# Kernel tuning notes

Hardware: AMD Instinct MI355X
Metric: run time of the kernel (lower is better)

The kernel has to match this reference:

```python
import jax, jax.numpy as jnp
import numpy as np

Q, N, FDIM, HDIM = 4096, 1024, 64, 128


def setup_inputs() -> dict:
    key = jax.random.key(0)
    ks = jax.random.split(key, 7)
    s = 0.05
    return {
        "query_points": jax.random.normal(ks[0], (Q, 3), dtype=jnp.float32),
        "node_features": jax.random.normal(ks[1], (N, FDIM), dtype=jnp.float32),
        "node_positions": jax.random.normal(ks[2], (N, 3), dtype=jnp.float32),
        # attention MLP: Linear(F+3 -> H), ReLU, Linear(H -> 1)
        "aW1": jax.random.normal(ks[3], (FDIM + 3, HDIM), dtype=jnp.float32) * s,
        "ab1": jnp.zeros((HDIM,), dtype=jnp.float32),
        "aW2": jax.random.normal(ks[4], (HDIM, 1), dtype=jnp.float32) * s,
        "ab2": jnp.zeros((1,), dtype=jnp.float32),
        # decoder MLP: Linear(F -> H), ReLU, Linear(H -> 3)
        "dW1": jax.random.normal(ks[5], (FDIM, HDIM), dtype=jnp.float32) * s,
        "db1": jnp.zeros((HDIM,), dtype=jnp.float32),
        "dW2": jax.random.normal(ks[6], (HDIM, 3), dtype=jnp.float32) * s,
        "db2": jnp.zeros((3,), dtype=jnp.float32),
    }


def reference(query_points, node_features, node_positions,
              aW1, ab1, aW2, ab2, dW1, db1, dW2, db2):
    F = node_features.shape[1]
    # pairwise offsets: [Q, N, 3]
    diff = query_points[:, None, :] - node_positions[None, :, :]
    # xy-plane distance -> inverse-distance weights: [Q, N, 1]
    dist = jnp.linalg.norm(diff[..., :2], axis=-1, keepdims=True)
    w = 1.0 / (dist + 1e-6)
    # attn MLP on concat([node_features, diff]); split W1 so the feature
    # part ([N,F]@[F,H]) is computed once instead of per query pair.
    h = jax.nn.relu(node_features @ aW1[:F] + diff @ aW1[F:] + ab1)  # [Q, N, H]
    score = h @ aW2 + ab2                                            # [Q, N, 1]
    attn = jax.nn.softmax(score * w, axis=1)                         # [Q, N, 1]
    agg = jnp.einsum('qn,nf->qf', attn[..., 0], node_features)       # [Q, F]
    return jax.nn.relu(agg @ dW1 + db1) @ dW2 + db2                  # [Q, 3]
```

## Files before the change

kernel.cpp:

```cpp
#include <hip/hip_runtime.h>
#include <math.h>

#define QN 4096
#define NN 1024
#define FD 64
#define HD 128

typedef float v2f __attribute__((ext_vector_type(2)));

#define OFF_UT2   0
#define OFF_B     524288
#define OFF_VU    655360
#define OFF_VB    659456
#define OFF_L     660480
#define OFF_PM    4854784
#define OFF_PART  5116928
#define OFF_SPART 7214080

__global__ __launch_bounds__(256) void k0_prep(
    const float* __restrict__ qp, const float* __restrict__ nf,
    const float* __restrict__ npos, const float* __restrict__ aW1,
    const float* __restrict__ ab1, const float* __restrict__ aW2,
    float* __restrict__ B, float* __restrict__ UT2,
    float* __restrict__ vu, float* __restrict__ vb) {
  int bid = blockIdx.x, t = threadIdx.x;
  if (bid < 2048) {
    int idx = bid * 256 + t;
    int e = idx & 1, q = (idx >> 1) & 4095, h2 = idx >> 13;
    int h = h2 * 2 + e;
    float u = qp[q*3+0] * aW1[(FD+0)*HD + h]
            + qp[q*3+1] * aW1[(FD+1)*HD + h]
            + qp[q*3+2] * aW1[(FD+2)*HD + h];
    UT2[idx] = u;
  } else if (bid < 2560) {
    int i2 = (bid - 2048) * 256 + t;
    int n = i2 >> 7, h = i2 & 127;
    float s = ab1[h];
    #pragma unroll
    for (int f = 0; f < FD; ++f) s = fmaf(nf[n*FD+f], aW1[f*HD+h], s);
    s -= npos[n*3+0] * aW1[(FD+0)*HD + h]
       + npos[n*3+1] * aW1[(FD+1)*HD + h]
       + npos[n*3+2] * aW1[(FD+2)*HD + h];
    B[i2] = s;
    float pv = s * aW2[h];
    #pragma unroll
    for (int m = 1; m < 64; m <<= 1) pv += __shfl_xor(pv, m, 64);
    __shared__ float ps[4];
    if ((t & 63) == 0) ps[t >> 6] = pv;
    __syncthreads();
    if (t == 0)   vb[n] = ps[0] + ps[1];
    if (t == 128) vb[n] = ps[2] + ps[3];
  } else {
    int q = (bid - 2560) * 256 + t;
    float q0 = qp[q*3+0], q1 = qp[q*3+1], q2 = qp[q*3+2];
    float acc = 0.f;
    #pragma unroll
    for (int h = 0; h < HD; ++h) {
      float u = q0 * aW1[(FD+0)*HD + h]
              + q1 * aW1[(FD+1)*HD + h]
              + q2 * aW1[(FD+2)*HD + h];
      acc = fmaf(aW2[h], u, acc);
    }
    vu[q] = acc;
  }
}

__global__ __launch_bounds__(256) void k2_logits(
    const float* __restrict__ Bg, const float* __restrict__ UT2,
    const float* __restrict__ aW2, const float* __restrict__ ab2,
    const float* __restrict__ qp, const float* __restrict__ npos,
    const float* __restrict__ vu, const float* __restrict__ vb,
    float* __restrict__ L, float* __restrict__ pm) {
  const int t = threadIdx.x;
  const int lane = t & 63, w = t >> 6;
  const int q = blockIdx.x * 256 + w * 64 + lane;
  const int n0 = blockIdx.y * 16;

  float acc[16];
  #pragma unroll
  for (int nn = 0; nn < 16; ++nn) acc[nn] = 0.f;

  const v2f* up = (const v2f*)UT2 + q;

  v2f uc[4], un[4];
  #pragma unroll
  for (int p = 0; p < 4; ++p) uc[p] = up[p * 4096];

  #pragma unroll 1
  for (int hc = 0; hc < 16; ++hc) {
    if (hc < 15) {
      const v2f* upn = up + (hc + 1) * 4 * 4096;
      #pragma unroll
      for (int p = 0; p < 4; ++p) un[p] = upn[p * 4096];
    }
    const float* awp = aW2 + hc * 8;
    float aw0 = awp[0], aw1 = awp[1], aw2 = awp[2], aw3 = awp[3];
    float aw4 = awp[4], aw5 = awp[5], aw6 = awp[6], aw7 = awp[7];
    #pragma unroll
    for (int nn = 0; nn < 16; ++nn) {
      const float* bp = Bg + (n0 + nn) * HD + hc * 8;
      float b0 = bp[0], b1 = bp[1], b2 = bp[2], b3 = bp[3];
      float b4 = bp[4], b5 = bp[5], b6 = bp[6], b7 = bp[7];
      float a = acc[nn];
      a = fmaf(aw0, __builtin_fabsf(uc[0].x + b0), a);
      a = fmaf(aw1, __builtin_fabsf(uc[0].y + b1), a);
      a = fmaf(aw2, __builtin_fabsf(uc[1].x + b2), a);
      a = fmaf(aw3, __builtin_fabsf(uc[1].y + b3), a);
      a = fmaf(aw4, __builtin_fabsf(uc[2].x + b4), a);
      a = fmaf(aw5, __builtin_fabsf(uc[2].y + b5), a);
      a = fmaf(aw6, __builtin_fabsf(uc[3].x + b6), a);
      a = fmaf(aw7, __builtin_fabsf(uc[3].y + b7), a);
      acc[nn] = a;
    }
    #pragma unroll
    for (int p = 0; p < 4; ++p) uc[p] = un[p];
  }

  const float bias2 = ab2[0];
  const float qx = qp[q*3+0], qy = qp[q*3+1];
  const float vuq = vu[q];
  float m = -3.4e38f;
  #pragma unroll
  for (int nn = 0; nn < 16; ++nn) {
    int n = n0 + nn;
    float px = npos[n*3+0], py = npos[n*3+1];
    float vbn = vb[n];
    float dx = qx - px, dy = qy - py;
    float wgt = 1.f / (sqrtf(dx*dx + dy*dy) + 1e-6f);
    float score = fmaf(0.5f, vuq + vbn + acc[nn], bias2);
    float lg = score * wgt;
    L[n * QN + q] = lg;
    m = fmaxf(m, lg);
  }
  pm[blockIdx.y * QN + q] = m;
}

__global__ __launch_bounds__(256) void k4_agg(
    const float* __restrict__ L, const float* __restrict__ pm,
    const float* __restrict__ nf, float* __restrict__ part,
    float* __restrict__ spart) {
  __shared__ float red[4][2][32][33];
  __shared__ float sred[4][33];
  int b = blockIdx.x;
  int qt = b & 127, c = b >> 7;
  int t = threadIdx.x, lane = t & 63, w = t >> 6;
  int qi = lane & 31, fh = lane >> 5;
  int q = qt * 32 + qi;

  float m = -3.4e38f;
  #pragma unroll
  for (int k = 0; k < 64; ++k) m = fmaxf(m, pm[k * QN + q]);

  float acc[32];
  #pragma unroll
  for (int f = 0; f < 32; ++f) acc[f] = 0.f;
  float s = 0.f;

  int nbase = c * 128 + w * 32;
  const float* Lp = L + (size_t)nbase * QN + q;
  float cur = *Lp;
  for (int i = 0; i < 32; ++i) {
    float nxt = (i < 31) ? Lp[(size_t)(i + 1) * QN] : 0.f;
    float p = exp2f((cur - m) * 1.44269504088896f);
    s += p;
    const float4* nfr = (const float4*)(nf + (nbase + i) * FD + fh * 32);
    #pragma unroll
    for (int g = 0; g < 8; ++g) {
      float4 a = nfr[g];
      acc[g*4+0] = fmaf(p, a.x, acc[g*4+0]);
      acc[g*4+1] = fmaf(p, a.y, acc[g*4+1]);
      acc[g*4+2] = fmaf(p, a.z, acc[g*4+2]);
      acc[g*4+3] = fmaf(p, a.w, acc[g*4+3]);
    }
    cur = nxt;
  }

  #pragma unroll
  for (int fi = 0; fi < 32; ++fi) red[w][fh][fi][qi] = acc[fi];
  if (fh == 0) sred[w][qi] = s;
  __syncthreads();
  #pragma unroll
  for (int k = 0; k < 8; ++k) {
    int idx = k * 256 + t;
    int qq = idx >> 6, f = idx & 63;
    int f1 = f >> 5, f0 = f & 31;
    float sum = red[0][f1][f0][qq] + red[1][f1][f0][qq]
              + red[2][f1][f0][qq] + red[3][f1][f0][qq];
    part[((size_t)c * QN + qt*32 + qq) * 64 + f] = sum;
  }
  if (t < 32) {
    spart[c * QN + qt*32 + t] = sred[0][t] + sred[1][t] + sred[2][t] + sred[3][t];
  }
}

__global__ __launch_bounds__(256) void k5_dec(
    const float* __restrict__ part, const float* __restrict__ spart,
    const float* __restrict__ dW1, const float* __restrict__ db1,
    const float* __restrict__ dW2, const float* __restrict__ db2,
    float* __restrict__ out) {
  __shared__ float agg[16][64];
  __shared__ float inv[16];
  __shared__ float h1s[16][128];
  int t = threadIdx.x;
  int qb = blockIdx.x * 16;
  if (t < 16) {
    float s = 0.f;
    #pragma unroll
    for (int c = 0; c < 8; ++c) s += spart[c*QN + qb + t];
    inv[t] = 1.f / s;
  }
  {
    int f = t & 63, qh = t >> 6;
    #pragma unroll
    for (int pass = 0; pass < 4; ++pass) {
      int qs = pass*4 + qh;
      float v = 0.f;
      #pragma unroll
      for (int c = 0; c < 8; ++c) v += part[((size_t)c*QN + qb + qs)*64 + f];
      agg[qs][f] = v;
    }
  }
  __syncthreads();
  {
    int h = t & 127, qg = t >> 7;
    #pragma unroll
    for (int k = 0; k < 8; ++k) {
      int qs = qg*8 + k;
      float a = 0.f;
      #pragma unroll
      for (int f = 0; f < 64; ++f) a = fmaf(agg[qs][f], dW1[f*HD + h], a);
      h1s[qs][h] = fmaxf(a * inv[qs] + db1[h], 0.f);
    }
  }
  __syncthreads();
  if (t < 48) {
    int qs = t / 3, o = t % 3;
    float a = db2[o];
    #pragma unroll
    for (int h = 0; h < HD; ++h) a = fmaf(h1s[qs][h], dW2[h*3 + o], a);
    out[(qb + qs)*3 + o] = a;
  }
}

extern "C" void kernel_launch(void* const* d_in, const int* in_sizes, int n_in,
                              void* d_out, int out_size, void* d_ws, size_t ws_size,
                              hipStream_t stream) {
  const float* qp   = (const float*)d_in[0];
  const float* nf   = (const float*)d_in[1];
  const float* npos = (const float*)d_in[2];
  const float* aW1  = (const float*)d_in[3];
  const float* ab1  = (const float*)d_in[4];
  const float* aW2  = (const float*)d_in[5];
  const float* ab2  = (const float*)d_in[6];
  const float* dW1  = (const float*)d_in[7];
  const float* db1  = (const float*)d_in[8];
  const float* dW2  = (const float*)d_in[9];
  const float* db2  = (const float*)d_in[10];

  float* ws    = (float*)d_ws;
  float* UT2   = ws + OFF_UT2;
  float* B     = ws + OFF_B;
  float* vu    = ws + OFF_VU;
  float* vb    = ws + OFF_VB;
  float* L     = ws + OFF_L;
  float* pm    = ws + OFF_PM;
  float* part  = ws + OFF_PART;
  float* spart = ws + OFF_SPART;

  hipLaunchKernelGGL(k0_prep, dim3(2576), dim3(256), 0, stream,
                     qp, nf, npos, aW1, ab1, aW2, B, UT2, vu, vb);
  hipLaunchKernelGGL(k2_logits, dim3(16, 64), dim3(256), 0, stream,
                     B, UT2, aW2, ab2, qp, npos, vu, vb, L, pm);
  hipLaunchKernelGGL(k4_agg, dim3(1024), dim3(256), 0, stream, L, pm, nf, part, spart);
  hipLaunchKernelGGL(k5_dec, dim3(256), dim3(256), 0, stream,
                     part, spart, dW1, db1, dW2, db2, (float*)d_out);
}
```

Measured before the change: 107.3 us.

## Fuse four kernels into one persistent kernel with grid-wide barriers

Replaces the four separate launches (prep, logits, aggregation, decoder) with a single persistent kernel of 512 blocks. The blocks loop over the work items of each former kernel and synchronise between stages with an atomic-counter grid barrier, which is reset by a memset before launch. The aim is to remove inter-kernel launch gaps and tail idle time. In exchange it adds spin-wait barriers, relies on all 512 blocks being co-resident to avoid deadlock, and runs stages with fewer blocks than before (the logits stage previously had 1024).

```diff
diff --git a/kernel.cpp b/kernel.cpp
--- a/kernel.cpp
+++ b/kernel.cpp
@@ -5,6 +5,7 @@
 #define NN 1024
 #define FD 64
 #define HD 128
+#define NBLK 512
 
 typedef float v2f __attribute__((ext_vector_type(2)));
 
@@ -16,229 +17,245 @@
 #define OFF_PM    4854784
 #define OFF_PART  5116928
 #define OFF_SPART 7214080
-
-__global__ __launch_bounds__(256) void k0_prep(
+#define OFF_CNT   7246848
+
+struct SmemP2 { float red[4][2][32][33]; float sred[4][33]; };
+struct SmemP3 { float agg[8][64]; float inv[8]; float h1s[8][128]; };
+union Smem {
+  float ps[4];
+  SmemP2 p2;
+  SmemP3 p3;
+};
+
+__device__ inline void grid_barrier(unsigned* cnt, unsigned target) {
+  __syncthreads();
+  if (threadIdx.x == 0) {
+    __threadfence();
+    __hip_atomic_fetch_add(cnt, 1u, __ATOMIC_ACQ_REL, __HIP_MEMORY_SCOPE_AGENT);
+    while (__hip_atomic_load(cnt, __ATOMIC_ACQUIRE, __HIP_MEMORY_SCOPE_AGENT) < target) {
+      __builtin_amdgcn_s_sleep(8);
+    }
+    __threadfence();
+  }
+  __syncthreads();
+}
+
+__global__ __launch_bounds__(256) void fused_all(
     const float* __restrict__ qp, const float* __restrict__ nf,
     const float* __restrict__ npos, const float* __restrict__ aW1,
     const float* __restrict__ ab1, const float* __restrict__ aW2,
-    float* __restrict__ B, float* __restrict__ UT2,
-    float* __restrict__ vu, float* __restrict__ vb) {
-  int bid = blockIdx.x, t = threadIdx.x;
-  if (bid < 2048) {
-    int idx = bid * 256 + t;
-    int e = idx & 1, q = (idx >> 1) & 4095, h2 = idx >> 13;
-    int h = h2 * 2 + e;
-    float u = qp[q*3+0] * aW1[(FD+0)*HD + h]
-            + qp[q*3+1] * aW1[(FD+1)*HD + h]
-            + qp[q*3+2] * aW1[(FD+2)*HD + h];
-    UT2[idx] = u;
-  } else if (bid < 2560) {
-    int i2 = (bid - 2048) * 256 + t;
-    int n = i2 >> 7, h = i2 & 127;
-    float s = ab1[h];
-    #pragma unroll
-    for (int f = 0; f < FD; ++f) s = fmaf(nf[n*FD+f], aW1[f*HD+h], s);
-    s -= npos[n*3+0] * aW1[(FD+0)*HD + h]
-       + npos[n*3+1] * aW1[(FD+1)*HD + h]
-       + npos[n*3+2] * aW1[(FD+2)*HD + h];
-    B[i2] = s;
-    float pv = s * aW2[h];
-    #pragma unroll
-    for (int m = 1; m < 64; m <<= 1) pv += __shfl_xor(pv, m, 64);
-    __shared__ float ps[4];
-    if ((t & 63) == 0) ps[t >> 6] = pv;
-    __syncthreads();
-    if (t == 0)   vb[n] = ps[0] + ps[1];
-    if (t == 128) vb[n] = ps[2] + ps[3];
-  } else {
-    int q = (bid - 2560) * 256 + t;
-    float q0 = qp[q*3+0], q1 = qp[q*3+1], q2 = qp[q*3+2];
-    float acc = 0.f;
-    #pragma unroll
-    for (int h = 0; h < HD; ++h) {
-      float u = q0 * aW1[(FD+0)*HD + h]
-              + q1 * aW1[(FD+1)*HD + h]
-              + q2 * aW1[(FD+2)*HD + h];
-      acc = fmaf(aW2[h], u, acc);
-    }
-    vu[q] = acc;
-  }
-}
-
-__global__ __launch_bounds__(256) void k2_logits(
-    const float* __restrict__ Bg, const float* __restrict__ UT2,
-    const float* __restrict__ aW2, const float* __restrict__ ab2,
-    const float* __restrict__ qp, const float* __restrict__ npos,
-    const float* __restrict__ vu, const float* __restrict__ vb,
-    float* __restrict__ L, float* __restrict__ pm) {
+    const float* __restrict__ ab2, const float* __restrict__ dW1,
+    const float* __restrict__ db1, const float* __restrict__ dW2,
+    const float* __restrict__ db2,
+    float* __restrict__ UT2, float* __restrict__ B,
+    float* __restrict__ vu, float* __restrict__ vb,
+    float* __restrict__ L, float* __restrict__ pm,
+    float* __restrict__ part, float* __restrict__ spart,
+    unsigned* __restrict__ cnt, float* __restrict__ out) {
+  __shared__ Smem sm;
   const int t = threadIdx.x;
   const int lane = t & 63, w = t >> 6;
-  const int q = blockIdx.x * 256 + w * 64 + lane;
-  const int n0 = blockIdx.y * 16;
-
-  float acc[16];
-  #pragma unroll
-  for (int nn = 0; nn < 16; ++nn) acc[nn] = 0.f;
-
-  const v2f* up = (const v2f*)UT2 + q;
-
-  v2f uc[4], un[4];
-  #pragma unroll
-  for (int p = 0; p < 4; ++p) uc[p] = up[p * 4096];
-
-  #pragma unroll 1
-  for (int hc = 0; hc < 16; ++hc) {
-    if (hc < 15) {
-      const v2f* upn = up + (hc + 1) * 4 * 4096;
-      #pragma unroll
-      for (int p = 0; p < 4; ++p) un[p] = upn[p * 4096];
-    }
-    const float* awp = aW2 + hc * 8;
-    float aw0 = awp[0], aw1 = awp[1], aw2 = awp[2], aw3 = awp[3];
-    float aw4 = awp[4], aw5 = awp[5], aw6 = awp[6], aw7 = awp[7];
+
+  for (int bid = blockIdx.x; bid < 2576; bid += NBLK) {
+    if (bid < 2048) {
+      int idx = bid * 256 + t;
+      int e = idx & 1, q = (idx >> 1) & 4095, h2 = idx >> 13;
+      int h = h2 * 2 + e;
+      UT2[idx] = qp[q*3+0] * aW1[(FD+0)*HD + h]
+               + qp[q*3+1] * aW1[(FD+1)*HD + h]
+               + qp[q*3+2] * aW1[(FD+2)*HD + h];
+    } else if (bid < 2560) {
+      int i2 = (bid - 2048) * 256 + t;
+      int n = i2 >> 7, h = i2 & 127;
+      float s = ab1[h];
+      #pragma unroll
+      for (int f = 0; f < FD; ++f) s = fmaf(nf[n*FD+f], aW1[f*HD+h], s);
+      s -= npos[n*3+0] * aW1[(FD+0)*HD + h]
+         + npos[n*3+1] * aW1[(FD+1)*HD + h]
+         + npos[n*3+2] * aW1[(FD+2)*HD + h];
+      B[i2] = s;
+      float pv = s * aW2[h];
+      #pragma unroll
+      for (int m = 1; m < 64; m <<= 1) pv += __shfl_xor(pv, m, 64);
+      if ((t & 63) == 0) sm.ps[t >> 6] = pv;
+      __syncthreads();
+      if (t == 0)   vb[n] = sm.ps[0] + sm.ps[1];
+      if (t == 128) vb[n] = sm.ps[2] + sm.ps[3];
+      __syncthreads();
+    } else {
+      int q = (bid - 2560) * 256 + t;
+      float q0 = qp[q*3+0], q1 = qp[q*3+1], q2 = qp[q*3+2];
+      float acc = 0.f;
+      #pragma unroll
+      for (int h = 0; h < HD; ++h) {
+        float u = q0 * aW1[(FD+0)*HD + h]
+                + q1 * aW1[(FD+1)*HD + h]
+                + q2 * aW1[(FD+2)*HD + h];
+        acc = fmaf(aW2[h], u, acc);
+      }
+      vu[q] = acc;
+    }
+  }
+  grid_barrier(cnt, NBLK);
+
+  for (int tile = blockIdx.x; tile < 1024; tile += NBLK) {
+    const int q = (tile & 15) * 256 + w * 64 + lane;
+    const int n0 = (tile >> 4) * 16;
+
+    float acc[16];
+    #pragma unroll
+    for (int nn = 0; nn < 16; ++nn) acc[nn] = 0.f;
+
+    const v2f* up = (const v2f*)UT2 + q;
+
+    v2f uc[4], un[4];
+    #pragma unroll
+    for (int p = 0; p < 4; ++p) uc[p] = up[p * 4096];
+
+    #pragma unroll 1
+    for (int hc = 0; hc < 16; ++hc) {
+      if (hc < 15) {
+        const v2f* upn = up + (hc + 1) * 4 * 4096;
+        #pragma unroll
+        for (int p = 0; p < 4; ++p) un[p] = upn[p * 4096];
+      }
+      const float* awp = aW2 + hc * 8;
+      float aw0 = awp[0], aw1 = awp[1], aw2 = awp[2], aw3 = awp[3];
+      float aw4 = awp[4], aw5 = awp[5], aw6 = awp[6], aw7 = awp[7];
+      #pragma unroll
+      for (int nn = 0; nn < 16; ++nn) {
+        const float* bp = B + (n0 + nn) * HD + hc * 8;
+        float b0 = bp[0], b1 = bp[1], b2 = bp[2], b3 = bp[3];
+        float b4 = bp[4], b5 = bp[5], b6 = bp[6], b7 = bp[7];
+        float a = acc[nn];
+        a = fmaf(aw0, __builtin_fabsf(uc[0].x + b0), a);
+        a = fmaf(aw1, __builtin_fabsf(uc[0].y + b1), a);
+        a = fmaf(aw2, __builtin_fabsf(uc[1].x + b2), a);
+        a = fmaf(aw3, __builtin_fabsf(uc[1].y + b3), a);
+        a = fmaf(aw4, __builtin_fabsf(uc[2].x + b4), a);
+        a = fmaf(aw5, __builtin_fabsf(uc[2].y + b5), a);
+        a = fmaf(aw6, __builtin_fabsf(uc[3].x + b6), a);
+        a = fmaf(aw7, __builtin_fabsf(uc[3].y + b7), a);
+        acc[nn] = a;
+      }
+      #pragma unroll
+      for (int p = 0; p < 4; ++p) uc[p] = un[p];
+    }
+
+    const float bias2 = ab2[0];
+    const float qx = qp[q*3+0], qy = qp[q*3+1];
+    const float vuq = vu[q];
+    float m = -3.4e38f;
     #pragma unroll
     for (int nn = 0; nn < 16; ++nn) {
-      const float* bp = Bg + (n0 + nn) * HD + hc * 8;
-      float b0 = bp[0], b1 = bp[1], b2 = bp[2], b3 = bp[3];
-      float b4 = bp[4], b5 = bp[5], b6 = bp[6], b7 = bp[7];
-      float a = acc[nn];
-      a = fmaf(aw0, __builtin_fabsf(uc[0].x + b0), a);
-      a = fmaf(aw1, __builtin_fabsf(uc[0].y + b1), a);
-      a = fmaf(aw2, __builtin_fabsf(uc[1].x + b2), a);
-      a = fmaf(aw3, __builtin_fabsf(uc[1].y + b3), a);
-      a = fmaf(aw4, __builtin_fabsf(uc[2].x + b4), a);
-      a = fmaf(aw5, __builtin_fabsf(uc[2].y + b5), a);
-      a = fmaf(aw6, __builtin_fabsf(uc[3].x + b6), a);
-      a = fmaf(aw7, __builtin_fabsf(uc[3].y + b7), a);
-      acc[nn] = a;
-    }
-    #pragma unroll
-    for (int p = 0; p < 4; ++p) uc[p] = un[p];
-  }
-
-  const float bias2 = ab2[0];
-  const float qx = qp[q*3+0], qy = qp[q*3+1];
-  const float vuq = vu[q];
-  float m = -3.4e38f;
-  #pragma unroll
-  for (int nn = 0; nn < 16; ++nn) {
-    int n = n0 + nn;
-    float px = npos[n*3+0], py = npos[n*3+1];
-    float vbn = vb[n];
-    float dx = qx - px, dy = qy - py;
-    float wgt = 1.f / (sqrtf(dx*dx + dy*dy) + 1e-6f);
-    float score = fmaf(0.5f, vuq + vbn + acc[nn], bias2);
-    float lg = score * wgt;
-    L[n * QN + q] = lg;
-    m = fmaxf(m, lg);
-  }
-  pm[blockIdx.y * QN + q] = m;
-}
-
-__global__ __launch_bounds__(256) void k4_agg(
-    const float* __restrict__ L, const float* __restrict__ pm,
-    const float* __restrict__ nf, float* __restrict__ part,
-    float* __restrict__ spart) {
-  __shared__ float red[4][2][32][33];
-  __shared__ float sred[4][33];
-  int b = blockIdx.x;
-  int qt = b & 127, c = b >> 7;
-  int t = threadIdx.x, lane = t & 63, w = t >> 6;
-  int qi = lane & 31, fh = lane >> 5;
-  int q = qt * 32 + qi;
-
-  float m = -3.4e38f;
-  #pragma unroll
-  for (int k = 0; k < 64; ++k) m = fmaxf(m, pm[k * QN + q]);
-
-  float acc[32];
-  #pragma unroll
-  for (int f = 0; f < 32; ++f) acc[f] = 0.f;
-  float s = 0.f;
-
-  int nbase = c * 128 + w * 32;
-  const float* Lp = L + (size_t)nbase * QN + q;
-  float cur = *Lp;
-  for (int i = 0; i < 32; ++i) {
-    float nxt = (i < 31) ? Lp[(size_t)(i + 1) * QN] : 0.f;
-    float p = exp2f((cur - m) * 1.44269504088896f);
-    s += p;
-    const float4* nfr = (const float4*)(nf + (nbase + i) * FD + fh * 32);
-    #pragma unroll
-    for (int g = 0; g < 8; ++g) {
-      float4 a = nfr[g];
-      acc[g*4+0] = fmaf(p, a.x, acc[g*4+0]);
-      acc[g*4+1] = fmaf(p, a.y, acc[g*4+1]);
-      acc[g*4+2] = fmaf(p, a.z, acc[g*4+2]);
-      acc[g*4+3] = fmaf(p, a.w, acc[g*4+3]);
-    }
-    cur = nxt;
-  }
-
-  #pragma unroll
-  for (int fi = 0; fi < 32; ++fi) red[w][fh][fi][qi] = acc[fi];
-  if (fh == 0) sred[w][qi] = s;
-  __syncthreads();
-  #pragma unroll
-  for (int k = 0; k < 8; ++k) {
-    int idx = k * 256 + t;
-    int qq = idx >> 6, f = idx & 63;
-    int f1 = f >> 5, f0 = f & 31;
-    float sum = red[0][f1][f0][qq] + red[1][f1][f0][qq]
-              + red[2][f1][f0][qq] + red[3][f1][f0][qq];
-    part[((size_t)c * QN + qt*32 + qq) * 64 + f] = sum;
-  }
-  if (t < 32) {
-    spart[c * QN + qt*32 + t] = sred[0][t] + sred[1][t] + sred[2][t] + sred[3][t];
-  }
-}
-
-__global__ __launch_bounds__(256) void k5_dec(
-    const float* __restrict__ part, const float* __restrict__ spart,
-    const float* __restrict__ dW1, const float* __restrict__ db1,
-    const float* __restrict__ dW2, const float* __restrict__ db2,
-    float* __restrict__ out) {
-  __shared__ float agg[16][64];
-  __shared__ float inv[16];
-  __shared__ float h1s[16][128];
-  int t = threadIdx.x;
-  int qb = blockIdx.x * 16;
-  if (t < 16) {
+      int n = n0 + nn;
+      float px = npos[n*3+0], py = npos[n*3+1];
+      float vbn = vb[n];
+      float dx = qx - px, dy = qy - py;
+      float wgt = 1.f / (sqrtf(dx*dx + dy*dy) + 1e-6f);
+      float score = fmaf(0.5f, vuq + vbn + acc[nn], bias2);
+      float lg = score * wgt;
+      L[n * QN + q] = lg;
+      m = fmaxf(m, lg);
+    }
+    pm[(tile >> 4) * QN + q] = m;
+  }
+  grid_barrier(cnt, 2 * NBLK);
+
+  for (int b = blockIdx.x; b < 1024; b += NBLK) {
+    int qt = b & 127, c = b >> 7;
+    int qi = lane & 31, fh = lane >> 5;
+    int q = qt * 32 + qi;
+
+    float m = -3.4e38f;
+    #pragma unroll
+    for (int k = 0; k < 64; ++k) m = fmaxf(m, pm[k * QN + q]);
+
+    float acc[32];
+    #pragma unroll
+    for (int f = 0; f < 32; ++f) acc[f] = 0.f;
     float s = 0.f;
-    #pragma unroll
-    for (int c = 0; c < 8; ++c) s += spart[c*QN + qb + t];
-    inv[t] = 1.f / s;
-  }
+
+    int nbase = c * 128 + w * 32;
+    const float* Lp = L + (size_t)nbase * QN + q;
+    float cur = *Lp;
+    for (int i = 0; i < 32; ++i) {
+      float nxt = (i < 31) ? Lp[(size_t)(i + 1) * QN] : 0.f;
+      float p = exp2f((cur - m) * 1.44269504088896f);
+      s += p;
+      const float4* nfr = (const float4*)(nf + (nbase + i) * FD + fh * 32);
+      #pragma unroll
+      for (int g = 0; g < 8; ++g) {
+        float4 a = nfr[g];
+        acc[g*4+0] = fmaf(p, a.x, acc[g*4+0]);
+        acc[g*4+1] = fmaf(p, a.y, acc[g*4+1]);
+        acc[g*4+2] = fmaf(p, a.z, acc[g*4+2]);
+        acc[g*4+3] = fmaf(p, a.w, acc[g*4+3]);
+      }
+      cur = nxt;
+    }
+
+    __syncthreads();
+    #pragma unroll
+    for (int fi = 0; fi < 32; ++fi) sm.p2.red[w][fh][fi][qi] = acc[fi];
+    if (fh == 0) sm.p2.sred[w][qi] = s;
+    __syncthreads();
+    #pragma unroll
+    for (int k = 0; k < 8; ++k) {
+      int idx = k * 256 + t;
+      int qq = idx >> 6, f = idx & 63;
+      int f1 = f >> 5, f0 = f & 31;
+      float sum = sm.p2.red[0][f1][f0][qq] + sm.p2.red[1][f1][f0][qq]
+                + sm.p2.red[2][f1][f0][qq] + sm.p2.red[3][f1][f0][qq];
+      part[((size_t)c * QN + qt*32 + qq) * 64 + f] = sum;
+    }
+    if (t < 32) {
+      spart[c * QN + qt*32 + t] = sm.p2.sred[0][t] + sm.p2.sred[1][t]
+                                + sm.p2.sred[2][t] + sm.p2.sred[3][t];
+    }
+    __syncthreads();
+  }
+  grid_barrier(cnt, 3 * NBLK);
+
   {
-    int f = t & 63, qh = t >> 6;
-    #pragma unroll
-    for (int pass = 0; pass < 4; ++pass) {
-      int qs = pass*4 + qh;
-      float v = 0.f;
-      #pragma unroll
-      for (int c = 0; c < 8; ++c) v += part[((size_t)c*QN + qb + qs)*64 + f];
-      agg[qs][f] = v;
-    }
-  }
-  __syncthreads();
-  {
-    int h = t & 127, qg = t >> 7;
-    #pragma unroll
-    for (int k = 0; k < 8; ++k) {
-      int qs = qg*8 + k;
-      float a = 0.f;
-      #pragma unroll
-      for (int f = 0; f < 64; ++f) a = fmaf(agg[qs][f], dW1[f*HD + h], a);
-      h1s[qs][h] = fmaxf(a * inv[qs] + db1[h], 0.f);
-    }
-  }
-  __syncthreads();
-  if (t < 48) {
-    int qs = t / 3, o = t % 3;
-    float a = db2[o];
-    #pragma unroll
-    for (int h = 0; h < HD; ++h) a = fmaf(h1s[qs][h], dW2[h*3 + o], a);
-    out[(qb + qs)*3 + o] = a;
+    int qb = blockIdx.x * 8;
+    if (t < 8) {
+      float s = 0.f;
+      #pragma unroll
+      for (int c = 0; c < 8; ++c) s += spart[c*QN + qb + t];
+      sm.p3.inv[t] = 1.f / s;
+    }
+    {
+      int f = t & 63, qh = t >> 6;
+      #pragma unroll
+      for (int pass = 0; pass < 2; ++pass) {
+        int qs = pass*4 + qh;
+        float v = 0.f;
+        #pragma unroll
+        for (int c = 0; c < 8; ++c) v += part[((size_t)c*QN + qb + qs)*64 + f];
+        sm.p3.agg[qs][f] = v;
+      }
+    }
+    __syncthreads();
+    {
+      int h = t & 127, qg = t >> 7;
+      #pragma unroll
+      for (int k = 0; k < 4; ++k) {
+        int qs = qg*4 + k;
+        float a = 0.f;
+        #pragma unroll
+        for (int f = 0; f < 64; ++f) a = fmaf(sm.p3.agg[qs][f], dW1[f*HD + h], a);
+        sm.p3.h1s[qs][h] = fmaxf(a * sm.p3.inv[qs] + db1[h], 0.f);
+      }
+    }
+    __syncthreads();
+    if (t < 24) {
+      int qs = t / 3, o = t % 3;
+      float a = db2[o];
+      #pragma unroll
+      for (int h = 0; h < HD; ++h) a = fmaf(sm.p3.h1s[qs][h], dW2[h*3 + o], a);
+      out[(qb + qs)*3 + o] = a;
+    }
   }
 }
 
@@ -266,12 +283,11 @@
   float* pm    = ws + OFF_PM;
   float* part  = ws + OFF_PART;
   float* spart = ws + OFF_SPART;
-
-  hipLaunchKernelGGL(k0_prep, dim3(2576), dim3(256), 0, stream,
-                     qp, nf, npos, aW1, ab1, aW2, B, UT2, vu, vb);
-  hipLaunchKernelGGL(k2_logits, dim3(16, 64), dim3(256), 0, stream,
-                     B, UT2, aW2, ab2, qp, npos, vu, vb, L, pm);
-  hipLaunchKernelGGL(k4_agg, dim3(1024), dim3(256), 0, stream, L, pm, nf, part, spart);
-  hipLaunchKernelGGL(k5_dec, dim3(256), dim3(256), 0, stream,
-                     part, spart, dW1, db1, dW2, db2, (float*)d_out);
+  unsigned* cnt = (unsigned*)(ws + OFF_CNT);
+  float* out   = (float*)d_out;
+
+  hipMemsetAsync(cnt, 0, sizeof(unsigned), stream);
+  hipLaunchKernelGGL(fused_all, dim3(NBLK), dim3(256), 0, stream,
+                     qp, nf, npos, aW1, ab1, aW2, ab2, dW1, db1, dW2, db2,
+                     UT2, B, vu, vb, L, pm, part, spart, cnt, out);
 }
```

Result: slower. 388.4 us (+262.1%).
